# Performance work log

Hardware: AMD Instinct MI355X
Metric: run time of the kernel (lower is better)

## Reference

```python
import jax, jax.numpy as jnp
import numpy as np

B, S, E, H = 2, 2048, 768, 12
D = E // H  # head_dim = 64


def setup_inputs() -> dict:
    key = jax.random.key(0)
    ks = jax.random.split(key, 5)
    scale = 1.0 / np.sqrt(E)
    return {
        "x": jax.random.normal(ks[0], (B, S, E), dtype=jnp.float32),
        "Wq": jax.random.normal(ks[1], (E, E), dtype=jnp.float32) * scale,
        "bq": jnp.zeros((E,), dtype=jnp.float32),
        "Wk": jax.random.normal(ks[2], (E, E), dtype=jnp.float32) * scale,
        "bk": jnp.zeros((E,), dtype=jnp.float32),
        "Wv": jax.random.normal(ks[3], (E, E), dtype=jnp.float32) * scale,
        "bv": jnp.zeros((E,), dtype=jnp.float32),
        "Wo": jax.random.normal(ks[4], (E, E), dtype=jnp.float32) * scale,
        "bo": jnp.zeros((E,), dtype=jnp.float32),
    }


def reference(x, Wq, bq, Wk, bk, Wv, bv, Wo, bo):
    # Linear layers (torch nn.Linear: y = x @ W^T + b; here W stored as (E,E), use x @ W + b)
    q = (x @ Wq + bq).reshape(B, S, H, D).transpose(0, 2, 1, 3)  # (B,H,S,D)
    k = (x @ Wk + bk).reshape(B, S, H, D).transpose(0, 2, 1, 3)
    v = (x @ Wv + bv).reshape(B, S, H, D).transpose(0, 2, 1, 3)
    scores = jnp.einsum("bhqd,bhkd->bhqk", q, k) / jnp.sqrt(jnp.float32(D))
    weights = jax.nn.softmax(scores, axis=-1)  # (B,H,S,S) -- explicitly returned
    out = jnp.einsum("bhqk,bhkd->bhqd", weights, v)
    out = out.transpose(0, 2, 1, 3).reshape(B, S, E)
    output = out @ Wo + bo
    return (output, weights)
```

## Files before the change

kernel.cpp:

```cpp
#include <hip/hip_runtime.h>
#include <hip/hip_fp16.h>

#define B_ 2
#define S_ 2048
#define E_ 768
#define H_ 12
#define D_ 64
#define BS_ 4096

typedef _Float16 half8 __attribute__((ext_vector_type(8)));
typedef _Float16 half4 __attribute__((ext_vector_type(4)));
typedef float f32x4 __attribute__((ext_vector_type(4)));

#define EXP_C 0.18033688011112042f

__device__ __forceinline__ f32x4 mfma16(half8 a, half8 b, f32x4 c) {
    return __builtin_amdgcn_mfma_f32_16x16x32_f16(a, b, c, 0, 0, 0);
}

__device__ __forceinline__ void gll16(const void* g, void* s) {
    __builtin_amdgcn_global_load_lds((const __attribute__((address_space(1))) void*)g,
                                     (__attribute__((address_space(3))) void*)s, 16, 0, 0);
}

__global__ void prep_kernel(const float* __restrict__ x,
                            const float* __restrict__ W0, const float* __restrict__ W1,
                            const float* __restrict__ W2, const float* __restrict__ W3,
                            _Float16* __restrict__ Wt, _Float16* __restrict__ xh) {
    int z = blockIdx.z;
    if (z == 4) {
        int n = BS_ * E_;
        int stride = 24 * 24 * 256 * 4;
        for (int i = ((blockIdx.y * 24 + blockIdx.x) * 256 + threadIdx.x) * 4; i < n; i += stride) {
            float4 v = *reinterpret_cast<const float4*>(x + i);
            half4 o;
            o.x = (_Float16)v.x; o.y = (_Float16)v.y; o.z = (_Float16)v.z; o.w = (_Float16)v.w;
            *reinterpret_cast<half4*>(xh + i) = o;
        }
        return;
    }
    __shared__ float tile[32][33];
    const float* W = (z == 0) ? W0 : (z == 1) ? W1 : (z == 2) ? W2 : W3;
    _Float16* dst = Wt + (size_t)z * E_ * E_;
    int out0 = blockIdx.x * 32, in0 = blockIdx.y * 32;
    int tx = threadIdx.x & 31, ty = threadIdx.x >> 5;
    #pragma unroll
    for (int r = ty; r < 32; r += 8) tile[r][tx] = W[(size_t)(in0 + r) * E_ + out0 + tx];
    __syncthreads();
    #pragma unroll
    for (int r = ty; r < 32; r += 8) dst[(size_t)(out0 + r) * E_ + in0 + tx] = (_Float16)tile[tx][r];
}

__global__ __launch_bounds__(256) void qkv_kernel(const _Float16* __restrict__ xh,
                                                  const _Float16* __restrict__ Wt,
                                                  const float* __restrict__ bq, const float* __restrict__ bk,
                                                  const float* __restrict__ bv,
                                                  _Float16* __restrict__ qw, _Float16* __restrict__ kw,
                                                  _Float16* __restrict__ vT) {
    __shared__ __align__(16) _Float16 ldsA[2][128 * 32];
    __shared__ __align__(16) _Float16 ldsB[2][128 * 32];
    int n0 = blockIdx.x * 128;
    int m0 = blockIdx.y * 128;
    int mat = n0 / E_;
    int col0 = n0 - mat * E_;
    int tid = threadIdx.x;
    int lane = tid & 63, wv = tid >> 6;
    int l15 = lane & 15, lhi = lane >> 4;
    int wm = wv >> 1, wn = wv & 1;
    const _Float16* Am = xh + (size_t)m0 * E_;
    const _Float16* Bm = Wt + (size_t)mat * E_ * E_ + (size_t)col0 * E_;

    int srow = wv * 16 + (lane >> 2);
    int sc16 = lane & 3;

    auto stage = [&](int buf, int k0) {
        #pragma unroll
        for (int is = 0; is < 2; ++is) {
            int row = is * 64 + srow;
            int c = (sc16 ^ ((row >> 1) & 3)) << 4;
            gll16((const char*)(Am + (size_t)row * E_ + k0) + c, &ldsA[buf][is * 2048 + wv * 512]);
            gll16((const char*)(Bm + (size_t)row * E_ + k0) + c, &ldsB[buf][is * 2048 + wv * 512]);
        }
    };

    f32x4 acc[4][4];
    #pragma unroll
    for (int mi = 0; mi < 4; ++mi)
        #pragma unroll
        for (int nj = 0; nj < 4; ++nj) acc[mi][nj] = (f32x4){0.f, 0.f, 0.f, 0.f};

    stage(0, 0);
    __syncthreads();
    for (int t = 0; t < E_ / 32; ++t) {
        if (t + 1 < E_ / 32) stage((t + 1) & 1, (t + 1) * 32);
        const _Float16* At = ldsA[t & 1];
        const _Float16* Bt = ldsB[t & 1];
        half8 af[4], bf[4];
        #pragma unroll
        for (int mi = 0; mi < 4; ++mi) {
            int row = wm * 64 + mi * 16 + l15;
            af[mi] = *reinterpret_cast<const half8*>(At + row * 32 + ((lhi ^ ((row >> 1) & 3)) << 3));
        }
        #pragma unroll
        for (int nj = 0; nj < 4; ++nj) {
            int row = wn * 64 + nj * 16 + l15;
            bf[nj] = *reinterpret_cast<const half8*>(Bt + row * 32 + ((lhi ^ ((row >> 1) & 3)) << 3));
        }
        #pragma unroll
        for (int mi = 0; mi < 4; ++mi)
            #pragma unroll
            for (int nj = 0; nj < 4; ++nj) acc[mi][nj] = mfma16(af[mi], bf[nj], acc[mi][nj]);
        __syncthreads();
    }

    const float* bias = (mat == 0) ? bq : (mat == 1) ? bk : bv;
    #pragma unroll
    for (int nj = 0; nj < 4; ++nj) {
        int col = col0 + wn * 64 + nj * 16 + l15;
        int h = col >> 6, d = col & 63;
        float bsv = bias[col];
        #pragma unroll
        for (int mi = 0; mi < 4; ++mi) {
            #pragma unroll
            for (int r = 0; r < 4; ++r) {
                int token = m0 + wm * 64 + mi * 16 + lhi * 4 + r;
                int bb = token >> 11, s = token & (S_ - 1);
                _Float16 val = (_Float16)(acc[mi][nj][r] + bsv);
                if (mat == 0)      qw[(((size_t)bb * H_ + h) * S_ + s) * D_ + d] = val;
                else if (mat == 1) kw[(((size_t)bb * H_ + h) * S_ + s) * D_ + d] = val;
                else               vT[(((size_t)bb * H_ + h) * D_ + d) * S_ + s] = val;
            }
        }
    }
}

__global__ __launch_bounds__(256) void attn_kernel(const _Float16* __restrict__ qw,
                                                   const _Float16* __restrict__ kw,
                                                   const _Float16* __restrict__ vT,
                                                   float* __restrict__ wout,
                                                   _Float16* __restrict__ aout) {
    __shared__ __align__(16) _Float16 ldsK[2][64 * 64];
    __shared__ __align__(16) _Float16 ldsV[2][64 * 64];
    __shared__ __align__(16) _Float16 plds[4][16 * 64];
    int qt = blockIdx.x, h = blockIdx.y, bb = blockIdx.z;
    int tid = threadIdx.x;
    int lane = tid & 63, w = tid >> 6;
    int l15 = lane & 15, lhi = lane >> 4;
    int q0 = qt * 64 + 16 * w;
    size_t bh = (size_t)bb * H_ + h;
    const _Float16* qbase = qw + bh * S_ * D_;
    const _Float16* kbase = kw + bh * S_ * D_;
    const _Float16* vbase = vT + bh * D_ * S_;

    int srow = w * 8 + (lane >> 3);
    int sc16 = lane & 7;

    auto stageK = [&](int buf, int kt0) {
        #pragma unroll
        for (int is = 0; is < 2; ++is) {
            int row = is * 32 + srow;
            const char* src = (const char*)(kbase + (size_t)(kt0 + row) * D_) + ((sc16 ^ (row & 7)) << 4);
            gll16(src, &ldsK[buf][is * 2048 + w * 512]);
        }
    };
    auto stageV = [&](int buf, int kt0) {
        #pragma unroll
        for (int is = 0; is < 2; ++is) {
            int row = is * 32 + srow;
            const char* src = (const char*)(vbase + (size_t)row * S_ + kt0) + ((sc16 ^ (row & 7)) << 4);
            gll16(src, &ldsV[buf][is * 2048 + w * 512]);
        }
    };

    half8 qa[2];
    #pragma unroll
    for (int kf = 0; kf < 2; ++kf)
        qa[kf] = *reinterpret_cast<const half8*>(qbase + (size_t)(q0 + l15) * D_ + kf * 32 + lhi * 8);

    float lsum[4] = {0.f, 0.f, 0.f, 0.f};
    stageK(0, 0);
    __syncthreads();
    for (int kt = 0; kt < S_ / 64; ++kt) {
        if (kt + 1 < S_ / 64) stageK((kt + 1) & 1, (kt + 1) * 64);
        const _Float16* Kb = ldsK[kt & 1];
        #pragma unroll
        for (int nf = 0; nf < 4; ++nf) {
            f32x4 sacc = (f32x4){0.f, 0.f, 0.f, 0.f};
            int row = nf * 16 + l15;
            __builtin_amdgcn_s_setprio(1);
            #pragma unroll
            for (int kf = 0; kf < 2; ++kf) {
                half8 kb = *reinterpret_cast<const half8*>(Kb + row * 64 + (((kf * 4 + lhi) ^ (row & 7)) << 3));
                sacc = mfma16(qa[kf], kb, sacc);
            }
            __builtin_amdgcn_s_setprio(0);
            #pragma unroll
            for (int r = 0; r < 4; ++r) lsum[r] += exp2f(sacc[r] * EXP_C);
        }
        __syncthreads();
    }
    #pragma unroll
    for (int r = 0; r < 4; ++r) {
        float v = lsum[r];
        v += __shfl_xor(v, 1);
        v += __shfl_xor(v, 2);
        v += __shfl_xor(v, 4);
        v += __shfl_xor(v, 8);
        lsum[r] = 1.0f / v;
    }

    f32x4 oacc[4];
    #pragma unroll
    for (int df = 0; df < 4; ++df) oacc[df] = (f32x4){0.f, 0.f, 0.f, 0.f};
    float* wbase = wout + bh * (size_t)S_ * S_;

    stageK(0, 0);
    stageV(0, 0);
    __syncthreads();
    for (int kt = 0; kt < S_ / 64; ++kt) {
        if (kt + 1 < S_ / 64) { stageK((kt + 1) & 1, (kt + 1) * 64); stageV((kt + 1) & 1, (kt + 1) * 64); }
        const _Float16* Kb = ldsK[kt & 1];
        const _Float16* Vb = ldsV[kt & 1];
        #pragma unroll
        for (int nf = 0; nf < 4; ++nf) {
            f32x4 sacc = (f32x4){0.f, 0.f, 0.f, 0.f};
            int row = nf * 16 + l15;
            __builtin_amdgcn_s_setprio(1);
            #pragma unroll
            for (int kf = 0; kf < 2; ++kf) {
                half8 kb = *reinterpret_cast<const half8*>(Kb + row * 64 + (((kf * 4 + lhi) ^ (row & 7)) << 3));
                sacc = mfma16(qa[kf], kb, sacc);
            }
            __builtin_amdgcn_s_setprio(0);
            #pragma unroll
            for (int r = 0; r < 4; ++r) {
                float p = exp2f(sacc[r] * EXP_C) * lsum[r];
                int q = lhi * 4 + r;
                int k = nf * 16 + l15;
                __builtin_nontemporal_store(p, &wbase[(size_t)(q0 + q) * S_ + kt * 64 + k]);
                plds[w][q * 64 + (((k >> 3) ^ (q & 7)) << 3) + (k & 7)] = (_Float16)p;
            }
        }
        __builtin_amdgcn_s_setprio(1);
        #pragma unroll
        for (int ks = 0; ks < 2; ++ks) {
            half8 pa = *reinterpret_cast<const half8*>(&plds[w][l15 * 64 + (((ks * 4 + lhi) ^ (l15 & 7)) << 3)]);
            #pragma unroll
            for (int df = 0; df < 4; ++df) {
                int drow = df * 16 + l15;
                half8 vb = *reinterpret_cast<const half8*>(Vb + drow * 64 + (((ks * 4 + lhi) ^ (drow & 7)) << 3));
                oacc[df] = mfma16(pa, vb, oacc[df]);
            }
        }
        __builtin_amdgcn_s_setprio(0);
        __syncthreads();
    }

    #pragma unroll
    for (int df = 0; df < 4; ++df) {
        #pragma unroll
        for (int r = 0; r < 4; ++r) {
            int token = bb * S_ + q0 + lhi * 4 + r;
            aout[(size_t)token * E_ + h * D_ + df * 16 + l15] = (_Float16)(oacc[df][r]);
        }
    }
}

__global__ __launch_bounds__(256) void proj_kernel(const _Float16* __restrict__ ah,
                                                   const _Float16* __restrict__ Wto,
                                                   const float* __restrict__ bo,
                                                   float* __restrict__ out) {
    __shared__ __align__(16) _Float16 ldsA[2][128 * 32];
    __shared__ __align__(16) _Float16 ldsB[2][128 * 32];
    int n0 = blockIdx.x * 128;
    int m0 = blockIdx.y * 128;
    int tid = threadIdx.x;
    int lane = tid & 63, wv = tid >> 6;
    int l15 = lane & 15, lhi = lane >> 4;
    int wm = wv >> 1, wn = wv & 1;
    const _Float16* Am = ah + (size_t)m0 * E_;
    const _Float16* Bm = Wto + (size_t)n0 * E_;

    int srow = wv * 16 + (lane >> 2);
    int sc16 = lane & 3;

    auto stage = [&](int buf, int k0) {
        #pragma unroll
        for (int is = 0; is < 2; ++is) {
            int row = is * 64 + srow;
            int c = (sc16 ^ ((row >> 1) & 3)) << 4;
            gll16((const char*)(Am + (size_t)row * E_ + k0) + c, &ldsA[buf][is * 2048 + wv * 512]);
            gll16((const char*)(Bm + (size_t)row * E_ + k0) + c, &ldsB[buf][is * 2048 + wv * 512]);
        }
    };

    f32x4 acc[4][4];
    #pragma unroll
    for (int mi = 0; mi < 4; ++mi)
        #pragma unroll
        for (int nj = 0; nj < 4; ++nj) acc[mi][nj] = (f32x4){0.f, 0.f, 0.f, 0.f};

    stage(0, 0);
    __syncthreads();
    for (int t = 0; t < E_ / 32; ++t) {
        if (t + 1 < E_ / 32) stage((t + 1) & 1, (t + 1) * 32);
        const _Float16* At = ldsA[t & 1];
        const _Float16* Bt = ldsB[t & 1];
        half8 af[4], bf[4];
        #pragma unroll
        for (int mi = 0; mi < 4; ++mi) {
            int row = wm * 64 + mi * 16 + l15;
            af[mi] = *reinterpret_cast<const half8*>(At + row * 32 + ((lhi ^ ((row >> 1) & 3)) << 3));
        }
        #pragma unroll
        for (int nj = 0; nj < 4; ++nj) {
            int row = wn * 64 + nj * 16 + l15;
            bf[nj] = *reinterpret_cast<const half8*>(Bt + row * 32 + ((lhi ^ ((row >> 1) & 3)) << 3));
        }
        #pragma unroll
        for (int mi = 0; mi < 4; ++mi)
            #pragma unroll
            for (int nj = 0; nj < 4; ++nj) acc[mi][nj] = mfma16(af[mi], bf[nj], acc[mi][nj]);
        __syncthreads();
    }

    #pragma unroll
    for (int nj = 0; nj < 4; ++nj) {
        int col = n0 + wn * 64 + nj * 16 + l15;
        float bsv = bo[col];
        #pragma unroll
        for (int mi = 0; mi < 4; ++mi) {
            #pragma unroll
            for (int r = 0; r < 4; ++r) {
                int token = m0 + wm * 64 + mi * 16 + lhi * 4 + r;
                __builtin_nontemporal_store(acc[mi][nj][r] + bsv, &out[(size_t)token * E_ + col]);
            }
        }
    }
}

extern "C" void kernel_launch(void* const* d_in, const int* in_sizes, int n_in,
                              void* d_out, int out_size, void* d_ws, size_t ws_size,
                              hipStream_t stream) {
    const float* x  = (const float*)d_in[0];
    const float* Wq = (const float*)d_in[1];
    const float* bq = (const float*)d_in[2];
    const float* Wk = (const float*)d_in[3];
    const float* bk = (const float*)d_in[4];
    const float* Wv = (const float*)d_in[5];
    const float* bv = (const float*)d_in[6];
    const float* Wo = (const float*)d_in[7];
    const float* bo = (const float*)d_in[8];

    char* ws = (char*)d_ws;
    _Float16* xh   = (_Float16*)(ws);
    _Float16* Wt   = (_Float16*)(ws + 6291456);
    _Float16* qw   = (_Float16*)(ws + 11010048);
    _Float16* kw   = (_Float16*)(ws + 17301504);
    _Float16* vT   = (_Float16*)(ws + 23592960);
    _Float16* aout = (_Float16*)(ws + 29884416);
    (void)ws_size; (void)in_sizes; (void)n_in; (void)out_size;

    float* out  = (float*)d_out;
    float* wout = out + (size_t)BS_ * E_;

    prep_kernel<<<dim3(24, 24, 5), dim3(256), 0, stream>>>(x, Wq, Wk, Wv, Wo, Wt, xh);
    qkv_kernel<<<dim3(3 * E_ / 128, BS_ / 128), dim3(256), 0, stream>>>(xh, Wt, bq, bk, bv, qw, kw, vT);
    attn_kernel<<<dim3(S_ / 64, H_, B_), dim3(256), 0, stream>>>(qw, kw, vT, wout, aout);
    proj_kernel<<<dim3(E_ / 128, BS_ / 128), dim3(256), 0, stream>>>(aout, Wt + (size_t)3 * E_ * E_, bo, out);
}
```

Before: 237.4 us.

## Defer softmax normalization, transpose score MFMA, remap blocks, narrow proj tiles

```diff
diff --git a/kernel.cpp b/kernel.cpp
--- a/kernel.cpp
+++ b/kernel.cpp
@@ -142,7 +142,10 @@
     __shared__ __align__(16) _Float16 ldsK[2][64 * 64];
     __shared__ __align__(16) _Float16 ldsV[2][64 * 64];
     __shared__ __align__(16) _Float16 plds[4][16 * 64];
-    int qt = blockIdx.x, h = blockIdx.y, bb = blockIdx.z;
+    int dsp = blockIdx.x;
+    int wk = (dsp & 7) * 96 + (dsp >> 3);
+    int qt = wk & 31, hb = wk >> 5;
+    int h = hb % H_, bb = hb / H_;
     int tid = threadIdx.x;
     int lane = tid & 63, w = tid >> 6;
     int l15 = lane & 15, lhi = lane >> 4;
@@ -177,42 +180,10 @@
     for (int kf = 0; kf < 2; ++kf)
         qa[kf] = *reinterpret_cast<const half8*>(qbase + (size_t)(q0 + l15) * D_ + kf * 32 + lhi * 8);
 
-    float lsum[4] = {0.f, 0.f, 0.f, 0.f};
-    stageK(0, 0);
-    __syncthreads();
-    for (int kt = 0; kt < S_ / 64; ++kt) {
-        if (kt + 1 < S_ / 64) stageK((kt + 1) & 1, (kt + 1) * 64);
-        const _Float16* Kb = ldsK[kt & 1];
-        #pragma unroll
-        for (int nf = 0; nf < 4; ++nf) {
-            f32x4 sacc = (f32x4){0.f, 0.f, 0.f, 0.f};
-            int row = nf * 16 + l15;
-            __builtin_amdgcn_s_setprio(1);
-            #pragma unroll
-            for (int kf = 0; kf < 2; ++kf) {
-                half8 kb = *reinterpret_cast<const half8*>(Kb + row * 64 + (((kf * 4 + lhi) ^ (row & 7)) << 3));
-                sacc = mfma16(qa[kf], kb, sacc);
-            }
-            __builtin_amdgcn_s_setprio(0);
-            #pragma unroll
-            for (int r = 0; r < 4; ++r) lsum[r] += exp2f(sacc[r] * EXP_C);
-        }
-        __syncthreads();
-    }
-    #pragma unroll
-    for (int r = 0; r < 4; ++r) {
-        float v = lsum[r];
-        v += __shfl_xor(v, 1);
-        v += __shfl_xor(v, 2);
-        v += __shfl_xor(v, 4);
-        v += __shfl_xor(v, 8);
-        lsum[r] = 1.0f / v;
-    }
-
+    float lsum = 0.f;
     f32x4 oacc[4];
     #pragma unroll
     for (int df = 0; df < 4; ++df) oacc[df] = (f32x4){0.f, 0.f, 0.f, 0.f};
-    float* wbase = wout + bh * (size_t)S_ * S_;
 
     stageK(0, 0);
     stageV(0, 0);
@@ -224,27 +195,28 @@
         #pragma unroll
         for (int nf = 0; nf < 4; ++nf) {
             f32x4 sacc = (f32x4){0.f, 0.f, 0.f, 0.f};
-            int row = nf * 16 + l15;
+            int rowk = nf * 16 + l15;
             __builtin_amdgcn_s_setprio(1);
             #pragma unroll
             for (int kf = 0; kf < 2; ++kf) {
-                half8 kb = *reinterpret_cast<const half8*>(Kb + row * 64 + (((kf * 4 + lhi) ^ (row & 7)) << 3));
-                sacc = mfma16(qa[kf], kb, sacc);
+                half8 kb = *reinterpret_cast<const half8*>(Kb + rowk * 64 + (((kf * 4 + lhi) ^ (rowk & 7)) << 3));
+                sacc = mfma16(kb, qa[kf], sacc);
             }
             __builtin_amdgcn_s_setprio(0);
+            half4 pk;
             #pragma unroll
             for (int r = 0; r < 4; ++r) {
-                float p = exp2f(sacc[r] * EXP_C) * lsum[r];
-                int q = lhi * 4 + r;
-                int k = nf * 16 + l15;
-                __builtin_nontemporal_store(p, &wbase[(size_t)(q0 + q) * S_ + kt * 64 + k]);
-                plds[w][q * 64 + (((k >> 3) ^ (q & 7)) << 3) + (k & 7)] = (_Float16)p;
-            }
+                float p = exp2f(sacc[r] * EXP_C);
+                lsum += p;
+                pk[r] = (_Float16)p;
+            }
+            int ke = nf * 16 + lhi * 4;
+            *reinterpret_cast<half4*>(&plds[w][(l15 << 6) + ((((ke >> 3) ^ (l15 & 7)) << 3) | (ke & 7))]) = pk;
         }
         __builtin_amdgcn_s_setprio(1);
         #pragma unroll
         for (int ks = 0; ks < 2; ++ks) {
-            half8 pa = *reinterpret_cast<const half8*>(&plds[w][l15 * 64 + (((ks * 4 + lhi) ^ (l15 & 7)) << 3)]);
+            half8 pa = *reinterpret_cast<const half8*>(&plds[w][(l15 << 6) + (((ks * 4 + lhi) ^ (l15 & 7)) << 3)]);
             #pragma unroll
             for (int df = 0; df < 4; ++df) {
                 int drow = df * 16 + l15;
@@ -256,13 +228,45 @@
         __syncthreads();
     }
 
+    lsum += __shfl_xor(lsum, 16);
+    lsum += __shfl_xor(lsum, 32);
+    float rs = 1.0f / lsum;
+
+    float rsq[4];
+    #pragma unroll
+    for (int r = 0; r < 4; ++r) rsq[r] = __shfl(rs, lhi * 4 + r);
     #pragma unroll
     for (int df = 0; df < 4; ++df) {
         #pragma unroll
         for (int r = 0; r < 4; ++r) {
             int token = bb * S_ + q0 + lhi * 4 + r;
-            aout[(size_t)token * E_ + h * D_ + df * 16 + l15] = (_Float16)(oacc[df][r]);
-        }
+            aout[(size_t)token * E_ + h * D_ + df * 16 + l15] = (_Float16)(oacc[df][r] * rsq[r]);
+        }
+    }
+
+    float* wbase = wout + bh * (size_t)S_ * S_ + (size_t)(q0 + l15) * S_;
+    stageK(0, 0);
+    __syncthreads();
+    for (int kt = 0; kt < S_ / 64; ++kt) {
+        if (kt + 1 < S_ / 64) stageK((kt + 1) & 1, (kt + 1) * 64);
+        const _Float16* Kb = ldsK[kt & 1];
+        #pragma unroll
+        for (int nf = 0; nf < 4; ++nf) {
+            f32x4 sacc = (f32x4){0.f, 0.f, 0.f, 0.f};
+            int rowk = nf * 16 + l15;
+            __builtin_amdgcn_s_setprio(1);
+            #pragma unroll
+            for (int kf = 0; kf < 2; ++kf) {
+                half8 kb = *reinterpret_cast<const half8*>(Kb + rowk * 64 + (((kf * 4 + lhi) ^ (rowk & 7)) << 3));
+                sacc = mfma16(kb, qa[kf], sacc);
+            }
+            __builtin_amdgcn_s_setprio(0);
+            f32x4 pv;
+            #pragma unroll
+            for (int r = 0; r < 4; ++r) pv[r] = exp2f(sacc[r] * EXP_C) * rs;
+            __builtin_nontemporal_store(pv, reinterpret_cast<f32x4*>(&wbase[kt * 64 + nf * 16 + lhi * 4]));
+        }
+        __syncthreads();
     }
 }
 
@@ -271,8 +275,8 @@
                                                    const float* __restrict__ bo,
                                                    float* __restrict__ out) {
     __shared__ __align__(16) _Float16 ldsA[2][128 * 32];
-    __shared__ __align__(16) _Float16 ldsB[2][128 * 32];
-    int n0 = blockIdx.x * 128;
+    __shared__ __align__(16) _Float16 ldsB[2][64 * 32];
+    int n0 = blockIdx.x * 64;
     int m0 = blockIdx.y * 128;
     int tid = threadIdx.x;
     int lane = tid & 63, wv = tid >> 6;
@@ -290,15 +294,19 @@
             int row = is * 64 + srow;
             int c = (sc16 ^ ((row >> 1) & 3)) << 4;
             gll16((const char*)(Am + (size_t)row * E_ + k0) + c, &ldsA[buf][is * 2048 + wv * 512]);
-            gll16((const char*)(Bm + (size_t)row * E_ + k0) + c, &ldsB[buf][is * 2048 + wv * 512]);
+        }
+        {
+            int row = srow;
+            int c = (sc16 ^ ((row >> 1) & 3)) << 4;
+            gll16((const char*)(Bm + (size_t)row * E_ + k0) + c, &ldsB[buf][wv * 512]);
         }
     };
 
-    f32x4 acc[4][4];
+    f32x4 acc[4][2];
     #pragma unroll
     for (int mi = 0; mi < 4; ++mi)
         #pragma unroll
-        for (int nj = 0; nj < 4; ++nj) acc[mi][nj] = (f32x4){0.f, 0.f, 0.f, 0.f};
+        for (int nj = 0; nj < 2; ++nj) acc[mi][nj] = (f32x4){0.f, 0.f, 0.f, 0.f};
 
     stage(0, 0);
     __syncthreads();
@@ -306,27 +314,27 @@
         if (t + 1 < E_ / 32) stage((t + 1) & 1, (t + 1) * 32);
         const _Float16* At = ldsA[t & 1];
         const _Float16* Bt = ldsB[t & 1];
-        half8 af[4], bf[4];
+        half8 af[4], bf[2];
         #pragma unroll
         for (int mi = 0; mi < 4; ++mi) {
             int row = wm * 64 + mi * 16 + l15;
             af[mi] = *reinterpret_cast<const half8*>(At + row * 32 + ((lhi ^ ((row >> 1) & 3)) << 3));
         }
         #pragma unroll
-        for (int nj = 0; nj < 4; ++nj) {
-            int row = wn * 64 + nj * 16 + l15;
+        for (int nj = 0; nj < 2; ++nj) {
+            int row = wn * 32 + nj * 16 + l15;
             bf[nj] = *reinterpret_cast<const half8*>(Bt + row * 32 + ((lhi ^ ((row >> 1) & 3)) << 3));
         }
         #pragma unroll
         for (int mi = 0; mi < 4; ++mi)
             #pragma unroll
-            for (int nj = 0; nj < 4; ++nj) acc[mi][nj] = mfma16(af[mi], bf[nj], acc[mi][nj]);
+            for (int nj = 0; nj < 2; ++nj) acc[mi][nj] = mfma16(af[mi], bf[nj], acc[mi][nj]);
         __syncthreads();
     }
 
     #pragma unroll
-    for (int nj = 0; nj < 4; ++nj) {
-        int col = n0 + wn * 64 + nj * 16 + l15;
+    for (int nj = 0; nj < 2; ++nj) {
+        int col = n0 + wn * 32 + nj * 16 + l15;
         float bsv = bo[col];
         #pragma unroll
         for (int mi = 0; mi < 4; ++mi) {
@@ -366,6 +374,6 @@
 
     prep_kernel<<<dim3(24, 24, 5), dim3(256), 0, stream>>>(x, Wq, Wk, Wv, Wo, Wt, xh);
     qkv_kernel<<<dim3(3 * E_ / 128, BS_ / 128), dim3(256), 0, stream>>>(xh, Wt, bq, bk, bv, qw, kw, vT);
-    attn_kernel<<<dim3(S_ / 64, H_, B_), dim3(256), 0, stream>>>(qw, kw, vT, wout, aout);
-    proj_kernel<<<dim3(E_ / 128, BS_ / 128), dim3(256), 0, stream>>>(aout, Wt + (size_t)3 * E_ * E_, bo, out);
-}
+    attn_kernel<<<dim3(768), dim3(256), 0, stream>>>(qw, kw, vT, wout, aout);
+    proj_kernel<<<dim3(E_ / 64, BS_ / 128), dim3(256), 0, stream>>>(aout, Wt + (size_t)3 * E_ * E_, bo, out);
+}
```

Result: no change. 237.2 us, median of 2 (-0.1%).
